# Optimization experiments

Hardware: AMD Instinct MI355X
Metric: run time of the kernel (lower is better)

Reference implementation:

```python
import jax, jax.numpy as jnp
import numpy as np

EPS = 1e-5
NUM_HEADS = 8
KEY_DEPTH = 128   # base_filters * key_expansion
VAL_DEPTH = 256   # base_filters * value_expansion
C_IN = 256


def conv1x1(x, w):
    # x: [N, Cin, L], w: [Cout, Cin] (1x1 conv, no bias)
    return jnp.einsum('oc,ncl->nol', w, x)


def group_norm1(x, w, b, eps=EPS):
    # torch GroupNorm(1, C) on [N, C, L]: normalize over (C, L) per sample,
    # per-channel affine.
    mu = jnp.mean(x, axis=(1, 2), keepdims=True)
    var = jnp.var(x, axis=(1, 2), keepdims=True)
    xn = (x - mu) * jax.lax.rsqrt(var + eps)
    return xn * w[None, :, None] + b[None, :, None]


def layer_norm_last2(x, eps=EPS):
    # freshly-constructed nn.LayerNorm([A, B]): weight=1, bias=0 -> pure norm
    mu = jnp.mean(x, axis=(-2, -1), keepdims=True)
    var = jnp.var(x, axis=(-2, -1), keepdims=True)
    return (x - mu) * jax.lax.rsqrt(var + eps)


def gelu(x):
    return jax.nn.gelu(x, approximate=False)  # torch F.gelu default (erf)


def setup_inputs() -> dict:
    key = jax.random.key(0)
    ks = jax.random.split(key, 16)
    N, L = 8, 1024
    qkv_out = 2 * KEY_DEPTH + VAL_DEPTH  # 512

    def w(k, shape, std=0.02):
        return jax.random.normal(k, shape, jnp.float32) * std

    def gw(k, c):
        return 1.0 + 0.1 * jax.random.normal(k, (c,), jnp.float32)

    return {
        'f': jax.random.normal(ks[0], (N, C_IN, L), jnp.float32),
        'w_z': w(ks[1], (C_IN, C_IN), np.sqrt(2.0 / C_IN)),
        'gz_w': gw(ks[2], C_IN), 'gz_b': w(ks[3], (C_IN,)),
        'w_qkv': w(ks[4], (qkv_out, C_IN), C_IN ** -0.5),
        'gq_w': gw(ks[5], qkv_out), 'gq_b': w(ks[6], (qkv_out,)),
        'w_out': w(ks[7], (C_IN, VAL_DEPTH), np.sqrt(2.0 / VAL_DEPTH)),
        'go_w': gw(ks[8], C_IN), 'go_b': w(ks[9], (C_IN,)),
        'w_ffn1': w(ks[10], (2 * C_IN, C_IN), np.sqrt(2.0 / C_IN)),
        'g1_w': gw(ks[11], 2 * C_IN), 'g1_b': w(ks[12], (2 * C_IN,)),
        'w_ffn2': w(ks[13], (C_IN, 2 * C_IN), np.sqrt(1.0 / C_IN)),
        'g2_w': gw(ks[14], C_IN), 'g2_b': w(ks[15], (C_IN,)),
    }


def reference(f, w_z, gz_w, gz_b, w_qkv, gq_w, gq_b, w_out, go_w, go_b,
              w_ffn1, g1_w, g1_b, w_ffn2, g2_w, g2_b):
    N, C, L = f.shape
    H = NUM_HEADS

    z = gelu(group_norm1(conv1x1(gelu(f), w_z), gz_w, gz_b))
    qkv = group_norm1(conv1x1(z, w_qkv), gq_w, gq_b)
    q, k, v = jnp.split(qkv, [KEY_DEPTH, 2 * KEY_DEPTH], axis=1)
    q = q.reshape(N, H, KEY_DEPTH // H, L)
    k = k.reshape(N, H, KEY_DEPTH // H, L)
    v = v.reshape(N, H, VAL_DEPTH // H, L)

    # [N, H, L, L] similarity, no scaling, then LayerNorm over full LxL map
    logits = jnp.einsum('nhcl,nhcm->nhlm', q, k)
    logits = layer_norm_last2(logits)

    # scatter-mask: diagonal -> -inf for every head
    eye = jnp.eye(L, dtype=bool)[None, None]  # [1,1,L,L]
    logits = jnp.where(eye, -jnp.inf, logits)

    attn = jax.nn.softmax(logits.astype(jnp.float32), axis=-1)
    attn = jnp.where(jnp.isnan(attn), 0.0, attn)

    out = jnp.einsum('nhlm,nhdm->nhdl', attn, v).reshape(N, VAL_DEPTH, L)
    out = gelu(layer_norm_last2(out))  # LayerNorm([C_v, L]), fresh params

    out = group_norm1(conv1x1(out, w_out), go_w, go_b)
    f = gelu(f + out)

    h = gelu(group_norm1(conv1x1(f, w_ffn1), g1_w, g1_b))
    h = group_norm1(conv1x1(h, w_ffn2), g2_w, g2_b)
    return gelu(f + h)
```

## Files before the change

kernel.cpp:

```cpp
#include <hip/hip_runtime.h>

#define LSEQ 1024

typedef __attribute__((ext_vector_type(8))) short bf16x8;
typedef __attribute__((ext_vector_type(4))) float f32x4;

__device__ __forceinline__ float gelu_f(float x){
    return 0.5f*x*(1.0f+erff(x*0.7071067811865476f));
}

__device__ __forceinline__ unsigned f2bf1(float x){
    unsigned u = __float_as_uint(x);
    return (u + 0x7fffu + ((u>>16)&1u)) >> 16;
}
__device__ __forceinline__ unsigned packbf(float lo, float hi){
    return f2bf1(lo) | (f2bf1(hi)<<16);
}

__global__ __launch_bounds__(256,2) void prologue(
    const float* __restrict__ w0, const float* __restrict__ w1,
    const float* __restrict__ w2, const float* __restrict__ w3,
    const float* __restrict__ w4, unsigned short* __restrict__ wdst,
    const float* __restrict__ f, unsigned short* __restrict__ t0,
    float* __restrict__ stats, float* __restrict__ covs)
{
    __shared__ float T[64][68];
    int b = blockIdx.x;
    int tid = threadIdx.x;

    if(b < 512){
        int ltile = (b&15)*64, ctile = ((b>>4)&3)*64, n = b>>6;
        const float* s = f + (size_t)n*256*LSEQ;
        int cl = tid>>4, l4 = (tid&15)*4;
        #pragma unroll
        for(int p=0;p<4;p++){
            int c_loc = p*16 + cl;
            float4 v = *(const float4*)&s[(size_t)(ctile+c_loc)*LSEQ + ltile + l4];
            float4 t;
            t.x = gelu_f(v.x); t.y = gelu_f(v.y); t.z = gelu_f(v.z); t.w = gelu_f(v.w);
            *(float4*)&T[c_loc][l4] = t;
        }
        __syncthreads();
        int l_loc = tid>>2, cg = (tid&3)*16;
        uint4 o0, o1;
        o0.x = packbf(T[cg+0][l_loc],  T[cg+1][l_loc]);
        o0.y = packbf(T[cg+2][l_loc],  T[cg+3][l_loc]);
        o0.z = packbf(T[cg+4][l_loc],  T[cg+5][l_loc]);
        o0.w = packbf(T[cg+6][l_loc],  T[cg+7][l_loc]);
        o1.x = packbf(T[cg+8][l_loc],  T[cg+9][l_loc]);
        o1.y = packbf(T[cg+10][l_loc], T[cg+11][l_loc]);
        o1.z = packbf(T[cg+12][l_loc], T[cg+13][l_loc]);
        o1.w = packbf(T[cg+14][l_loc], T[cg+15][l_loc]);
        unsigned short* d = t0 + (size_t)n*LSEQ*256 + (size_t)(ltile+l_loc)*256 + ctile + cg;
        *(uint4*)d = o0;
        *(uint4*)(d+8) = o1;
    } else if(b < 1024){
        int idx4 = (b-512)*256 + tid;
        const float* src; int off4;
        if(idx4 < 16384){ src=w0; off4=idx4; }
        else if(idx4 < 49152){ src=w1; off4=idx4-16384; }
        else if(idx4 < 65536){ src=w2; off4=idx4-49152; }
        else if(idx4 < 98304){ src=w3; off4=idx4-65536; }
        else { src=w4; off4=idx4-98304; }
        float4 v = ((const float4*)src)[off4];
        uint2 p; p.x = packbf(v.x,v.y); p.y = packbf(v.z,v.w);
        ((uint2*)wdst)[idx4] = p;
    } else if(b == 1024){
        if(tid < 64) ((float4*)stats)[tid] = (float4){0.f,0.f,0.f,0.f};
    } else {
        int i = (b-1025)*256 + tid;
        ((float4*)covs)[i] = (float4){0.f,0.f,0.f,0.f};
    }
}

__global__ __launch_bounds__(256,2) void xform_bf16(
    const float* __restrict__ src, const float* __restrict__ res,
    const float* __restrict__ stats,
    const float* __restrict__ gw, const float* __restrict__ gb,
    float cnt_inv, int C, unsigned short* __restrict__ dst)
{
    __shared__ float T[64][68];
    int n = blockIdx.z;
    int ltile = blockIdx.x*64, ctile = blockIdx.y*64;
    int tid = threadIdx.x;

    float mu=0.f, istd=1.f;
    if(stats){
        float s1 = stats[2*n], s2 = stats[2*n+1];
        mu = s1*cnt_inv;
        istd = rsqrtf(s2*cnt_inv - mu*mu + 1e-5f);
    }
    const float* s = src + (size_t)n*C*LSEQ;
    const float* r = res ? res + (size_t)n*C*LSEQ : nullptr;

    int cl = tid>>4, l4 = (tid&15)*4;
    #pragma unroll
    for(int p=0;p<4;p++){
        int c_loc = p*16 + cl;
        int c = ctile + c_loc;
        float w_ = 1.f, b_ = 0.f;
        if(stats){ w_ = istd; b_ = -mu*istd; }
        if(gw){ b_ = gb[c] + b_*gw[c]; w_ *= gw[c]; }
        float4 v = *(const float4*)&s[(size_t)c*LSEQ + ltile + l4];
        float4 t;
        t.x = v.x*w_+b_; t.y = v.y*w_+b_; t.z = v.z*w_+b_; t.w = v.w*w_+b_;
        if(r){
            float4 rv = *(const float4*)&r[(size_t)c*LSEQ + ltile + l4];
            t.x += rv.x; t.y += rv.y; t.z += rv.z; t.w += rv.w;
        }
        t.x = gelu_f(t.x); t.y = gelu_f(t.y); t.z = gelu_f(t.z); t.w = gelu_f(t.w);
        *(float4*)&T[c_loc][l4] = t;
    }
    __syncthreads();

    int l_loc = tid>>2, cg = (tid&3)*16;
    uint4 o0, o1;
    o0.x = packbf(T[cg+0][l_loc],  T[cg+1][l_loc]);
    o0.y = packbf(T[cg+2][l_loc],  T[cg+3][l_loc]);
    o0.z = packbf(T[cg+4][l_loc],  T[cg+5][l_loc]);
    o0.w = packbf(T[cg+6][l_loc],  T[cg+7][l_loc]);
    o1.x = packbf(T[cg+8][l_loc],  T[cg+9][l_loc]);
    o1.y = packbf(T[cg+10][l_loc], T[cg+11][l_loc]);
    o1.z = packbf(T[cg+12][l_loc], T[cg+13][l_loc]);
    o1.w = packbf(T[cg+14][l_loc], T[cg+15][l_loc]);
    unsigned short* d = dst + (size_t)n*LSEQ*C + (size_t)(ltile+l_loc)*C + ctile + cg;
    *(uint4*)d = o0;
    *(uint4*)(d+8) = o1;
}

__global__ __launch_bounds__(256,2) void gemm_bf16(
    const unsigned short* __restrict__ Abf,
    const unsigned short* __restrict__ Bbf,
    float* __restrict__ C,
    int M, int K,
    float* __restrict__ out_stats)
{
    __shared__ short As[64*264];
    __shared__ short Bs[64*264];

    int tid = threadIdx.x;
    int n = blockIdx.z, n0 = blockIdx.x*64, m0 = blockIdx.y*64;
    int wave = tid>>6, lane = tid&63;
    int col = lane&15, quad = lane>>4;
    int srow = tid>>2, sks = (tid&3)*8;

    const unsigned short* apt = Abf + (size_t)(m0+srow)*K + sks;
    const unsigned short* bpt = Bbf + ((size_t)n*LSEQ + n0+srow)*K + sks;

    f32x4 acc[4];
    #pragma unroll
    for(int t=0;t<4;t++) acc[t] = (f32x4){0.f,0.f,0.f,0.f};

    for(int kp=0; kp<K; kp+=256){
        __syncthreads();
        uint4 av[8], bw[8];
        #pragma unroll
        for(int i=0;i<8;i++) av[i] = *(const uint4*)(apt + kp + i*32);
        #pragma unroll
        for(int i=0;i<8;i++) bw[i] = *(const uint4*)(bpt + kp + i*32);
        #pragma unroll
        for(int i=0;i<8;i++) *(uint4*)&As[srow*264 + sks + i*32] = av[i];
        #pragma unroll
        for(int i=0;i<8;i++) *(uint4*)&Bs[srow*264 + sks + i*32] = bw[i];
        __syncthreads();

        #pragma unroll
        for(int kc=0;kc<8;kc++){
            bf16x8 af = *(bf16x8*)&As[(wave*16+col)*264 + kc*32 + quad*8];
            #pragma unroll
            for(int t=0;t<4;t++){
                bf16x8 bf = *(bf16x8*)&Bs[(t*16+col)*264 + kc*32 + quad*8];
                acc[t] = __builtin_amdgcn_mfma_f32_16x16x32_bf16(af, bf, acc[t], 0,0,0);
            }
        }
    }

    __syncthreads();
    size_t cbase = (size_t)n*M*LSEQ;
    float lsum=0.f, lsq=0.f;
    #pragma unroll
    for(int t=0;t<4;t++){
        #pragma unroll
        for(int r2=0;r2<4;r2++){
            int m = m0 + wave*16 + quad*4 + r2;
            int l = n0 + t*16 + col;
            float v = acc[t][r2];
            C[cbase + (size_t)m*LSEQ + l] = v;
            lsum += v; lsq += v*v;
        }
    }
    float* scr = (float*)As;
    scr[tid] = lsum; scr[256+tid] = lsq;
    __syncthreads();
    for(int s=128;s>0;s>>=1){
        if(tid<s){ scr[tid]+=scr[tid+s]; scr[256+tid]+=scr[256+tid+s]; }
        __syncthreads();
    }
    if(tid==0){
        atomicAdd(&out_stats[2*n],   scr[0]);
        atomicAdd(&out_stats[2*n+1], scr[256]);
    }
}

__global__ __launch_bounds__(256,2) void head_cov(
    const float* __restrict__ qkv,
    const float* __restrict__ s_qkv,
    const float* __restrict__ gq_w, const float* __restrict__ gq_b,
    float* __restrict__ covq, float* __restrict__ covk,
    float* __restrict__ sumq, float* __restrict__ sumk)
{
    __shared__ float Kq[16*132];
    __shared__ float Kk[16*132];
    int b = blockIdx.x;
    int head = b>>3, chunk = b&7;
    int n = head>>3, h = head&7;
    int tid = threadIdx.x;
    int m0 = chunk*128;

    float s1 = s_qkv[2*n], s2v = s_qkv[2*n+1];
    float mu  = s1*(1.f/524288.f);
    float var = s2v*(1.f/524288.f) - mu*mu;
    float istd = rsqrtf(var + 1e-5f);

    const float* base = qkv + (size_t)n*512*LSEQ;
    int m = tid&127, cg = tid>>7;
    #pragma unroll
    for(int cc=0;cc<8;cc++){
        int c = cg*8+cc;
        int chq = h*16+c, chk = 128+h*16+c;
        Kq[c*132+m] = (base[(size_t)chq*LSEQ+m0+m]-mu)*istd*gq_w[chq]+gq_b[chq];
        Kk[c*132+m] = (base[(size_t)chk*LSEQ+m0+m]-mu)*istd*gq_w[chk]+gq_b[chk];
    }
    __syncthreads();

    int i = tid>>4, j = tid&15;
    float q0=0,q1=0,q2=0,q3=0, k0=0,k1=0,k2=0,k3=0;
    for(int mm=0;mm<128;mm+=4){
        float4 qa = *(const float4*)&Kq[i*132+mm];
        float4 qb = *(const float4*)&Kq[j*132+mm];
        q0 += qa.x*qb.x; q1 += qa.y*qb.y; q2 += qa.z*qb.z; q3 += qa.w*qb.w;
        float4 ka = *(const float4*)&Kk[i*132+mm];
        float4 kb = *(const float4*)&Kk[j*132+mm];
        k0 += ka.x*kb.x; k1 += ka.y*kb.y; k2 += ka.z*kb.z; k3 += ka.w*kb.w;
    }
    atomicAdd(&covq[head*256 + i*16 + j], (q0+q1)+(q2+q3));
    atomicAdd(&covk[head*256 + i*16 + j], (k0+k1)+(k2+k3));

    if(i==0){
        float s=0.f;
        for(int mm=0;mm<128;mm+=4){
            float4 v = *(const float4*)&Kq[j*132+mm];
            s += (v.x+v.y)+(v.z+v.w);
        }
        atomicAdd(&sumq[head*16+j], s);
    }
    if(i==1){
        float s=0.f;
        for(int mm=0;mm<128;mm+=4){
            float4 v = *(const float4*)&Kk[j*132+mm];
            s += (v.x+v.y)+(v.z+v.w);
        }
        atomicAdd(&sumk[head*16+j], s);
    }
}

__global__ __launch_bounds__(256) void attn_kernel(
    const float* __restrict__ qkv,
    const float* __restrict__ s_qkv,
    const float* __restrict__ gq_w, const float* __restrict__ gq_b,
    const float* __restrict__ covq, const float* __restrict__ covk,
    const float* __restrict__ sumq, const float* __restrict__ sumk,
    float* __restrict__ out,
    float* __restrict__ out_stats)
{
    __shared__ short Qs[128*40];
    __shared__ short Ks[128*40];
    __shared__ short Vs[32*136];
    __shared__ short Ps[128*152];
    __shared__ float bounds_l[128];
    __shared__ float issum_l[128];
    __shared__ float sred4[4];

    int b = blockIdx.x;
    int head = b&63, rb = b>>6;
    int n = head>>3, h = head&7;
    int tid = threadIdx.x;
    int wv = tid>>6, lane = tid&63;
    int col = lane&15, quad = lane>>4;
    int l0 = rb*128;

    float ih;
    {
        float* fs = (float*)Ps;
        fs[tid] = covq[head*256+tid]*covk[head*256+tid];
        __syncthreads();
        for(int s=128;s>0;s>>=1){
            if(tid<s) fs[tid]+=fs[tid+s];
            __syncthreads();
        }
        if(tid==0){
            double S2 = (double)fs[0];
            double S1 = 0.0;
            for(int c=0;c<16;c++)
                S1 += (double)sumq[head*16+c]*(double)sumk[head*16+c];
            double cnt = 1048576.0;
            double mean = S1/cnt;
            double v2 = S2/cnt - mean*mean;
            if(v2 < 0.0) v2 = 0.0;
            fs[0] = (float)(1.0/sqrt(v2 + 1e-5));
        }
        __syncthreads();
        ih = fs[0];
        __syncthreads();
    }

    const float* base = qkv + (size_t)n*512*LSEQ;
    float s1 = s_qkv[2*n], s2v = s_qkv[2*n+1];
    float mu  = s1*(1.f/524288.f);
    float var = s2v*(1.f/524288.f) - mu*mu;
    float istd = rsqrtf(var + 1e-5f);

    {
        int row = tid>>1, hf = tid&1;
        uint4 z = {0,0,0,0};
        *(uint4*)&Qs[row*40 + 16 + hf*8] = z;
        *(uint4*)&Ks[row*40 + 16 + hf*8] = z;
    }

    {
        int row = tid>>1, cg = tid&1;
        float qn2p = 0.f;
        float qv[8];
        #pragma unroll
        for(int cc=0;cc<8;cc++){
            int ch = h*16 + cg*8 + cc;
            float w_ = gq_w[ch]*istd, b_ = gq_b[ch]-mu*istd*gq_w[ch];
            float x = base[(size_t)ch*LSEQ + l0 + row];
            float v = x*w_ + b_;
            qv[cc] = v;
            qn2p += v*v;
        }
        uint4 pq;
        pq.x = packbf(qv[0],qv[1]); pq.y = packbf(qv[2],qv[3]);
        pq.z = packbf(qv[4],qv[5]); pq.w = packbf(qv[6],qv[7]);
        *(uint4*)&Qs[row*40 + cg*8] = pq;
        float oth = __shfl_xor(qn2p, 1);
        if(cg==0) bounds_l[row] = sqrtf(qn2p + oth);
    }

    {
        float kn2max = 0.f;
        #pragma unroll
        for(int j=0;j<4;j++){
            int m = tid + j*256;
            float s = 0.f;
            for(int c=0;c<16;c++){
                int ch = 128+h*16+c;
                float x = base[(size_t)ch*LSEQ + m];
                float kv = (x-mu)*istd*gq_w[ch]+gq_b[ch];
                s += kv*kv;
            }
            kn2max = fmaxf(kn2max, s);
        }
        #pragma unroll
        for(int d=1;d<64;d<<=1) kn2max = fmaxf(kn2max, __shfl_xor(kn2max,d));
        if(lane==0) sred4[wv] = kn2max;
    }
    __syncthreads();
    float kmax = sqrtf(fmaxf(fmaxf(sred4[0],sred4[1]),fmaxf(sred4[2],sred4[3])));

    bf16x8 qf[2];
    float B2[2]; int grow[2];
    #pragma unroll
    for(int t=0;t<2;t++){
        int rl = (2*wv+t)*16 + col;
        qf[t] = *(bf16x8*)&Qs[rl*40 + quad*8];
        B2[t] = bounds_l[rl]*kmax*ih;
        grow[t] = l0 + rl;
    }

    int km_l = tid>>1, kg = tid&1;
    float kw8[8], kb8[8];
    #pragma unroll
    for(int cc=0;cc<8;cc++){
        int ch = 128+h*16+kg*8+cc;
        kw8[cc] = gq_w[ch]*istd;
        kb8[cc] = gq_b[ch]-mu*istd*gq_w[ch];
    }
    int vd = tid>>3, vmg = tid&7;
    float vw, vb;
    {
        int ch = 256+h*32+vd;
        vw = gq_w[ch]*istd;
        vb = gq_b[ch]-mu*istd*gq_w[ch];
    }
    const float* kp = base + (size_t)(128+h*16+kg*8)*LSEQ + km_l;
    const float* vp = base + (size_t)(256+h*32+vd)*LSEQ + vmg*16;

    f32x4 acc[2][2];
    #pragma unroll
    for(int t=0;t<2;t++){ acc[t][0]=(f32x4){0,0,0,0}; acc[t][1]=(f32x4){0,0,0,0}; }
    float ssum[2] = {0.f,0.f};
    const f32x4 zero4 = {0.f,0.f,0.f,0.f};

    for(int mc=0;mc<8;mc++){
        int M0 = mc*128;
        {
            float kv[8];
            #pragma unroll
            for(int cc=0;cc<8;cc++)
                kv[cc] = kp[(size_t)cc*LSEQ + M0]*kw8[cc] + kb8[cc];
            uint4 pk;
            pk.x=packbf(kv[0],kv[1]); pk.y=packbf(kv[2],kv[3]);
            pk.z=packbf(kv[4],kv[5]); pk.w=packbf(kv[6],kv[7]);
            *(uint4*)&Ks[km_l*40 + kg*8] = pk;
        }
        {
            float4 x0 = *(const float4*)&vp[M0];
            float4 x1 = *(const float4*)&vp[M0+4];
            float4 x2 = *(const float4*)&vp[M0+8];
            float4 x3 = *(const float4*)&vp[M0+12];
            uint4 p0, p1;
            p0.x = packbf(x0.x*vw+vb, x0.y*vw+vb);
            p0.y = packbf(x0.z*vw+vb, x0.w*vw+vb);
            p0.z = packbf(x1.x*vw+vb, x1.y*vw+vb);
            p0.w = packbf(x1.z*vw+vb, x1.w*vw+vb);
            p1.x = packbf(x2.x*vw+vb, x2.y*vw+vb);
            p1.y = packbf(x2.z*vw+vb, x2.w*vw+vb);
            p1.z = packbf(x3.x*vw+vb, x3.y*vw+vb);
            p1.w = packbf(x3.z*vw+vb, x3.w*vw+vb);
            *(uint4*)&Vs[vd*136 + vmg*16]     = p0;
            *(uint4*)&Vs[vd*136 + vmg*16 + 8] = p1;
        }
        __syncthreads();

        #pragma unroll
        for(int mt=0;mt<8;mt++){
            bf16x8 ak = *(bf16x8*)&Ks[(mt*16+col)*40 + quad*8];
            #pragma unroll
            for(int t=0;t<2;t++){
                f32x4 sc = __builtin_amdgcn_mfma_f32_16x16x32_bf16(ak, qf[t], zero4, 0,0,0);
                int mbase = M0 + mt*16 + quad*4;
                float pr[4];
                #pragma unroll
                for(int r=0;r<4;r++){
                    float e = __expf(fmaf(sc[r], ih, -B2[t]));
                    pr[r] = (mbase + r == grow[t]) ? 0.f : e;
                    ssum[t] += pr[r];
                }
                uint2 pw;
                pw.x = packbf(pr[0],pr[1]); pw.y = packbf(pr[2],pr[3]);
                *(uint2*)&Ps[((2*wv+t)*16+col)*152 + mt*16 + quad*4] = pw;
            }
        }
        #pragma unroll
        for(int kk=0;kk<4;kk++){
            bf16x8 bv0 = *(bf16x8*)&Vs[( col)*136 + kk*32 + quad*8];
            bf16x8 bv1 = *(bf16x8*)&Vs[((16+col))*136 + kk*32 + quad*8];
            #pragma unroll
            for(int t=0;t<2;t++){
                bf16x8 ap = *(bf16x8*)&Ps[((2*wv+t)*16+col)*152 + kk*32 + quad*8];
                acc[t][0] = __builtin_amdgcn_mfma_f32_16x16x32_bf16(ap, bv0, acc[t][0], 0,0,0);
                acc[t][1] = __builtin_amdgcn_mfma_f32_16x16x32_bf16(ap, bv1, acc[t][1], 0,0,0);
            }
        }
        __syncthreads();
    }

    #pragma unroll
    for(int t=0;t<2;t++){
        float v = ssum[t];
        v += __shfl_xor(v,16);
        v += __shfl_xor(v,32);
        if(quad==0) issum_l[(2*wv+t)*16+col] = v;
    }
    __syncthreads();
    if(tid<128) issum_l[tid] = 1.f/issum_l[tid];
    __syncthreads();

    float* ep = (float*)Ps;
    #pragma unroll
    for(int t=0;t<2;t++)
        #pragma unroll
        for(int dt=0;dt<2;dt++)
            *(f32x4*)&ep[(dt*16+col)*132 + (2*wv+t)*16 + quad*4] = acc[t][dt];
    __syncthreads();

    float lsum=0.f, lsq=0.f;
    size_t obase = (size_t)n*262144 + (size_t)h*32*LSEQ + l0;
    #pragma unroll
    for(int t=0;t<16;t++){
        int idx = t*256 + tid;
        int d = idx>>7, row = idx&127;
        float y = ep[d*132+row]*issum_l[row];
        out[obase + (size_t)d*LSEQ + row] = y;
        lsum += y; lsq += y*y;
    }
    float* red = (float*)Ks;
    red[tid]=lsum; red[256+tid]=lsq;
    __syncthreads();
    for(int s=128;s>0;s>>=1){
        if(tid<s){ red[tid]+=red[tid+s]; red[256+tid]+=red[256+tid+s]; }
        __syncthreads();
    }
    if(tid==0){
        atomicAdd(&out_stats[2*n],   red[0]);
        atomicAdd(&out_stats[2*n+1], red[256]);
    }
}

__global__ __launch_bounds__(256) void ew_final(
    const float* __restrict__ f, const float* __restrict__ x,
    const float* __restrict__ h2,
    const float* __restrict__ sx, const float* __restrict__ sh,
    const float* __restrict__ go_w, const float* __restrict__ go_b,
    const float* __restrict__ g2_w, const float* __restrict__ g2_b,
    float* __restrict__ out)
{
    int idx = blockIdx.x*256 + threadIdx.x;
    int n = idx >> 16;
    int c = (idx >> 8) & 255;
    float mux, isx, muh, ish;
    {
        float s1 = sx[2*n], s2 = sx[2*n+1];
        mux = s1*(1.f/262144.f);
        isx = rsqrtf(s2*(1.f/262144.f) - mux*mux + 1e-5f);
        float t1 = sh[2*n], t2 = sh[2*n+1];
        muh = t1*(1.f/262144.f);
        ish = rsqrtf(t2*(1.f/262144.f) - muh*muh + 1e-5f);
    }
    float wo = go_w[c]*isx, bo = go_b[c]-mux*isx*go_w[c];
    float w2 = g2_w[c]*ish, b2 = g2_b[c]-muh*ish*g2_w[c];
    float4 xv = ((const float4*)x)[idx];
    float4 fv = ((const float4*)f)[idx];
    float4 hv = ((const float4*)h2)[idx];
    float4 ov;
    float f1;
    f1 = gelu_f(fv.x + xv.x*wo+bo); ov.x = gelu_f(f1 + hv.x*w2+b2);
    f1 = gelu_f(fv.y + xv.y*wo+bo); ov.y = gelu_f(f1 + hv.y*w2+b2);
    f1 = gelu_f(fv.z + xv.z*wo+bo); ov.z = gelu_f(f1 + hv.z*w2+b2);
    f1 = gelu_f(fv.w + xv.w*wo+bo); ov.w = gelu_f(f1 + hv.w*w2+b2);
    ((float4*)out)[idx] = ov;
}

extern "C" void kernel_launch(void* const* d_in, const int* in_sizes, int n_in,
                              void* d_out, int out_size, void* d_ws, size_t ws_size,
                              hipStream_t stream) {
    const float* f     = (const float*)d_in[0];
    const float* w_z   = (const float*)d_in[1];
    const float* gz_w  = (const float*)d_in[2];
    const float* gz_b  = (const float*)d_in[3];
    const float* w_qkv = (const float*)d_in[4];
    const float* gq_w  = (const float*)d_in[5];
    const float* gq_b  = (const float*)d_in[6];
    const float* w_out = (const float*)d_in[7];
    const float* go_w  = (const float*)d_in[8];
    const float* go_b  = (const float*)d_in[9];
    const float* w_f1  = (const float*)d_in[10];
    const float* g1_w  = (const float*)d_in[11];
    const float* g1_b  = (const float*)d_in[12];
    const float* w_f2  = (const float*)d_in[13];
    const float* g2_w  = (const float*)d_in[14];
    const float* g2_b  = (const float*)d_in[15];

    float* ws = (float*)d_ws;
    float* stats = ws;
    float* s_z    = stats + 0;
    float* s_qkv  = stats + 16;
    float* s_attn = stats + 32;
    float* s_x    = stats + 48;
    float* s_h1   = stats + 64;
    float* s_h2   = stats + 80;

    float* qkvF = ws + 256;
    float* z0F  = qkvF + 4194304;
    float* xF   = z0F + 2097152;
    unsigned short* t0 = (unsigned short*)(xF + 2097152);
    unsigned short* t1 = t0 + 2097152;
    unsigned short* wp = t1 + 2097152;
    unsigned short* t4 = (unsigned short*)z0F;
    unsigned short* wp_z   = wp;
    unsigned short* wp_qkv = wp + 65536;
    unsigned short* wp_out = wp + 196608;
    unsigned short* wp_f1  = wp + 262144;
    unsigned short* wp_f2  = wp + 393216;

    float* covq = xF;
    float* covk = xF + 16384;
    float* sumq = xF + 32768;
    float* sumk = xF + 33792;

    float* outp = (float*)d_out;

    dim3 blk(256);
    prologue<<<1059,blk,0,stream>>>(w_z, w_qkv, w_out, w_f1, w_f2, wp,
        f, t0, stats, covq);
    gemm_bf16<<<dim3(16,4,8),blk,0,stream>>>(wp_z, t0, z0F, 256, 256, s_z);
    xform_bf16<<<dim3(16,4,8),blk,0,stream>>>(z0F, nullptr, s_z, gz_w, gz_b,
        1.f/262144.f, 256, t1);
    gemm_bf16<<<dim3(16,8,8),blk,0,stream>>>(wp_qkv, t1, qkvF, 512, 256, s_qkv);
    head_cov<<<512,blk,0,stream>>>(qkvF, s_qkv, gq_w, gq_b, covq, covk, sumq, sumk);
    attn_kernel<<<512,blk,0,stream>>>(qkvF, s_qkv, gq_w, gq_b,
        covq, covk, sumq, sumk, z0F, s_attn);
    xform_bf16<<<dim3(16,4,8),blk,0,stream>>>(z0F, nullptr, s_attn, nullptr, nullptr,
        1.f/262144.f, 256, t0);
    gemm_bf16<<<dim3(16,4,8),blk,0,stream>>>(wp_out, t0, xF, 256, 256, s_x);
    xform_bf16<<<dim3(16,4,8),blk,0,stream>>>(xF, f, s_x, go_w, go_b,
        1.f/262144.f, 256, t1);
    gemm_bf16<<<dim3(16,8,8),blk,0,stream>>>(wp_f1, t1, qkvF, 512, 256, s_h1);
    xform_bf16<<<dim3(16,8,8),blk,0,stream>>>(qkvF, nullptr, s_h1, g1_w, g1_b,
        1.f/524288.f, 512, t4);
    gemm_bf16<<<dim3(16,4,8),blk,0,stream>>>(wp_f2, t4, qkvF, 256, 512, s_h2);
    ew_final<<<2048,blk,0,stream>>>(f, xF, qkvF, s_x, s_h2,
        go_w, go_b, g2_w, g2_b, outp);
}
```

Before: 303.4 us.

## Use hardware bf16 pack, prefetch K/V tiles, wave-shuffle reductions, exp2 softmax

```diff
diff --git a/kernel.cpp b/kernel.cpp
--- a/kernel.cpp
+++ b/kernel.cpp
@@ -9,12 +9,10 @@
     return 0.5f*x*(1.0f+erff(x*0.7071067811865476f));
 }
 
-__device__ __forceinline__ unsigned f2bf1(float x){
-    unsigned u = __float_as_uint(x);
-    return (u + 0x7fffu + ((u>>16)&1u)) >> 16;
-}
-__device__ __forceinline__ unsigned packbf(float lo, float hi){
-    return f2bf1(lo) | (f2bf1(hi)<<16);
+__device__ __forceinline__ unsigned cvtpk(float lo, float hi){
+    unsigned r;
+    asm("v_cvt_pk_bf16_f32 %0, %1, %2" : "=v"(r) : "v"(lo), "v"(hi));
+    return r;
 }
 
 __global__ __launch_bounds__(256,2) void prologue(
@@ -43,14 +41,14 @@
         __syncthreads();
         int l_loc = tid>>2, cg = (tid&3)*16;
         uint4 o0, o1;
-        o0.x = packbf(T[cg+0][l_loc],  T[cg+1][l_loc]);
-        o0.y = packbf(T[cg+2][l_loc],  T[cg+3][l_loc]);
-        o0.z = packbf(T[cg+4][l_loc],  T[cg+5][l_loc]);
-        o0.w = packbf(T[cg+6][l_loc],  T[cg+7][l_loc]);
-        o1.x = packbf(T[cg+8][l_loc],  T[cg+9][l_loc]);
-        o1.y = packbf(T[cg+10][l_loc], T[cg+11][l_loc]);
-        o1.z = packbf(T[cg+12][l_loc], T[cg+13][l_loc]);
-        o1.w = packbf(T[cg+14][l_loc], T[cg+15][l_loc]);
+        o0.x = cvtpk(T[cg+0][l_loc],  T[cg+1][l_loc]);
+        o0.y = cvtpk(T[cg+2][l_loc],  T[cg+3][l_loc]);
+        o0.z = cvtpk(T[cg+4][l_loc],  T[cg+5][l_loc]);
+        o0.w = cvtpk(T[cg+6][l_loc],  T[cg+7][l_loc]);
+        o1.x = cvtpk(T[cg+8][l_loc],  T[cg+9][l_loc]);
+        o1.y = cvtpk(T[cg+10][l_loc], T[cg+11][l_loc]);
+        o1.z = cvtpk(T[cg+12][l_loc], T[cg+13][l_loc]);
+        o1.w = cvtpk(T[cg+14][l_loc], T[cg+15][l_loc]);
         unsigned short* d = t0 + (size_t)n*LSEQ*256 + (size_t)(ltile+l_loc)*256 + ctile + cg;
         *(uint4*)d = o0;
         *(uint4*)(d+8) = o1;
@@ -63,7 +61,7 @@
         else if(idx4 < 98304){ src=w3; off4=idx4-65536; }
         else { src=w4; off4=idx4-98304; }
         float4 v = ((const float4*)src)[off4];
-        uint2 p; p.x = packbf(v.x,v.y); p.y = packbf(v.z,v.w);
+        uint2 p; p.x = cvtpk(v.x,v.y); p.y = cvtpk(v.z,v.w);
         ((uint2*)wdst)[idx4] = p;
     } else if(b == 1024){
         if(tid < 64) ((float4*)stats)[tid] = (float4){0.f,0.f,0.f,0.f};
@@ -115,14 +113,14 @@
 
     int l_loc = tid>>2, cg = (tid&3)*16;
     uint4 o0, o1;
-    o0.x = packbf(T[cg+0][l_loc],  T[cg+1][l_loc]);
-    o0.y = packbf(T[cg+2][l_loc],  T[cg+3][l_loc]);
-    o0.z = packbf(T[cg+4][l_loc],  T[cg+5][l_loc]);
-    o0.w = packbf(T[cg+6][l_loc],  T[cg+7][l_loc]);
-    o1.x = packbf(T[cg+8][l_loc],  T[cg+9][l_loc]);
-    o1.y = packbf(T[cg+10][l_loc], T[cg+11][l_loc]);
-    o1.z = packbf(T[cg+12][l_loc], T[cg+13][l_loc]);
-    o1.w = packbf(T[cg+14][l_loc], T[cg+15][l_loc]);
+    o0.x = cvtpk(T[cg+0][l_loc],  T[cg+1][l_loc]);
+    o0.y = cvtpk(T[cg+2][l_loc],  T[cg+3][l_loc]);
+    o0.z = cvtpk(T[cg+4][l_loc],  T[cg+5][l_loc]);
+    o0.w = cvtpk(T[cg+6][l_loc],  T[cg+7][l_loc]);
+    o1.x = cvtpk(T[cg+8][l_loc],  T[cg+9][l_loc]);
+    o1.y = cvtpk(T[cg+10][l_loc], T[cg+11][l_loc]);
+    o1.z = cvtpk(T[cg+12][l_loc], T[cg+13][l_loc]);
+    o1.w = cvtpk(T[cg+14][l_loc], T[cg+15][l_loc]);
     unsigned short* d = dst + (size_t)n*LSEQ*C + (size_t)(ltile+l_loc)*C + ctile + cg;
     *(uint4*)d = o0;
     *(uint4*)(d+8) = o1;
@@ -175,7 +173,6 @@
         }
     }
 
-    __syncthreads();
     size_t cbase = (size_t)n*M*LSEQ;
     float lsum=0.f, lsq=0.f;
     #pragma unroll
@@ -189,16 +186,14 @@
             lsum += v; lsq += v*v;
         }
     }
-    float* scr = (float*)As;
-    scr[tid] = lsum; scr[256+tid] = lsq;
-    __syncthreads();
-    for(int s=128;s>0;s>>=1){
-        if(tid<s){ scr[tid]+=scr[tid+s]; scr[256+tid]+=scr[256+tid+s]; }
-        __syncthreads();
-    }
-    if(tid==0){
-        atomicAdd(&out_stats[2*n],   scr[0]);
-        atomicAdd(&out_stats[2*n+1], scr[256]);
+    #pragma unroll
+    for(int d=1;d<64;d<<=1){
+        lsum += __shfl_xor(lsum, d);
+        lsq  += __shfl_xor(lsq,  d);
+    }
+    if(lane==0){
+        atomicAdd(&out_stats[2*n],   lsum);
+        atomicAdd(&out_stats[2*n+1], lsq);
     }
 }
 
@@ -291,15 +286,14 @@
 
     float ih;
     {
-        float* fs = (float*)Ps;
-        fs[tid] = covq[head*256+tid]*covk[head*256+tid];
-        __syncthreads();
-        for(int s=128;s>0;s>>=1){
-            if(tid<s) fs[tid]+=fs[tid+s];
-            __syncthreads();
-        }
+        float prod = covq[head*256+tid]*covk[head*256+tid];
+        #pragma unroll
+        for(int d=1;d<64;d<<=1) prod += __shfl_xor(prod, d);
+        if(lane==0) sred4[wv] = prod;
+        __syncthreads();
         if(tid==0){
-            double S2 = (double)fs[0];
+            double S2 = (double)sred4[0] + (double)sred4[1]
+                      + (double)sred4[2] + (double)sred4[3];
             double S1 = 0.0;
             for(int c=0;c<16;c++)
                 S1 += (double)sumq[head*16+c]*(double)sumk[head*16+c];
@@ -307,12 +301,13 @@
             double mean = S1/cnt;
             double v2 = S2/cnt - mean*mean;
             if(v2 < 0.0) v2 = 0.0;
-            fs[0] = (float)(1.0/sqrt(v2 + 1e-5));
-        }
-        __syncthreads();
-        ih = fs[0];
-        __syncthreads();
-    }
+            sred4[0] = (float)(1.0/sqrt(v2 + 1e-5));
+        }
+        __syncthreads();
+        ih = sred4[0];
+        __syncthreads();
+    }
+    float ihl = ih * 1.4426950408889634f;
 
     const float* base = qkv + (size_t)n*512*LSEQ;
     float s1 = s_qkv[2*n], s2v = s_qkv[2*n+1];
@@ -341,8 +336,8 @@
             qn2p += v*v;
         }
         uint4 pq;
-        pq.x = packbf(qv[0],qv[1]); pq.y = packbf(qv[2],qv[3]);
-        pq.z = packbf(qv[4],qv[5]); pq.w = packbf(qv[6],qv[7]);
+        pq.x = cvtpk(qv[0],qv[1]); pq.y = cvtpk(qv[2],qv[3]);
+        pq.z = cvtpk(qv[4],qv[5]); pq.w = cvtpk(qv[6],qv[7]);
         *(uint4*)&Qs[row*40 + cg*8] = pq;
         float oth = __shfl_xor(qn2p, 1);
         if(cg==0) bounds_l[row] = sqrtf(qn2p + oth);
@@ -370,12 +365,12 @@
     float kmax = sqrtf(fmaxf(fmaxf(sred4[0],sred4[1]),fmaxf(sred4[2],sred4[3])));
 
     bf16x8 qf[2];
-    float B2[2]; int grow[2];
+    float B2l[2]; int grow[2];
     #pragma unroll
     for(int t=0;t<2;t++){
         int rl = (2*wv+t)*16 + col;
         qf[t] = *(bf16x8*)&Qs[rl*40 + quad*8];
-        B2[t] = bounds_l[rl]*kmax*ih;
+        B2l[t] = bounds_l[rl]*kmax*ihl;
         grow[t] = l0 + rl;
     }
 
@@ -403,53 +398,71 @@
     float ssum[2] = {0.f,0.f};
     const f32x4 zero4 = {0.f,0.f,0.f,0.f};
 
+    float kn[8];
+    float4 v0n, v1n, v2n, v3n;
+    #pragma unroll
+    for(int cc=0;cc<8;cc++) kn[cc] = kp[(size_t)cc*LSEQ];
+    v0n = *(const float4*)&vp[0];
+    v1n = *(const float4*)&vp[4];
+    v2n = *(const float4*)&vp[8];
+    v3n = *(const float4*)&vp[12];
+
     for(int mc=0;mc<8;mc++){
         int M0 = mc*128;
         {
-            float kv[8];
-            #pragma unroll
-            for(int cc=0;cc<8;cc++)
-                kv[cc] = kp[(size_t)cc*LSEQ + M0]*kw8[cc] + kb8[cc];
             uint4 pk;
-            pk.x=packbf(kv[0],kv[1]); pk.y=packbf(kv[2],kv[3]);
-            pk.z=packbf(kv[4],kv[5]); pk.w=packbf(kv[6],kv[7]);
+            pk.x = cvtpk(kn[0]*kw8[0]+kb8[0], kn[1]*kw8[1]+kb8[1]);
+            pk.y = cvtpk(kn[2]*kw8[2]+kb8[2], kn[3]*kw8[3]+kb8[3]);
+            pk.z = cvtpk(kn[4]*kw8[4]+kb8[4], kn[5]*kw8[5]+kb8[5]);
+            pk.w = cvtpk(kn[6]*kw8[6]+kb8[6], kn[7]*kw8[7]+kb8[7]);
             *(uint4*)&Ks[km_l*40 + kg*8] = pk;
         }
         {
-            float4 x0 = *(const float4*)&vp[M0];
-            float4 x1 = *(const float4*)&vp[M0+4];
-            float4 x2 = *(const float4*)&vp[M0+8];
-            float4 x3 = *(const float4*)&vp[M0+12];
             uint4 p0, p1;
-            p0.x = packbf(x0.x*vw+vb, x0.y*vw+vb);
-            p0.y = packbf(x0.z*vw+vb, x0.w*vw+vb);
-            p0.z = packbf(x1.x*vw+vb, x1.y*vw+vb);
-            p0.w = packbf(x1.z*vw+vb, x1.w*vw+vb);
-            p1.x = packbf(x2.x*vw+vb, x2.y*vw+vb);
-            p1.y = packbf(x2.z*vw+vb, x2.w*vw+vb);
-            p1.z = packbf(x3.x*vw+vb, x3.y*vw+vb);
-            p1.w = packbf(x3.z*vw+vb, x3.w*vw+vb);
+            p0.x = cvtpk(v0n.x*vw+vb, v0n.y*vw+vb);
+            p0.y = cvtpk(v0n.z*vw+vb, v0n.w*vw+vb);
+            p0.z = cvtpk(v1n.x*vw+vb, v1n.y*vw+vb);
+            p0.w = cvtpk(v1n.z*vw+vb, v1n.w*vw+vb);
+            p1.x = cvtpk(v2n.x*vw+vb, v2n.y*vw+vb);
+            p1.y = cvtpk(v2n.z*vw+vb, v2n.w*vw+vb);
+            p1.z = cvtpk(v3n.x*vw+vb, v3n.y*vw+vb);
+            p1.w = cvtpk(v3n.z*vw+vb, v3n.w*vw+vb);
             *(uint4*)&Vs[vd*136 + vmg*16]     = p0;
             *(uint4*)&Vs[vd*136 + vmg*16 + 8] = p1;
         }
         __syncthreads();
 
+        if(mc < 7){
+            int M1 = M0 + 128;
+            #pragma unroll
+            for(int cc=0;cc<8;cc++) kn[cc] = kp[(size_t)cc*LSEQ + M1];
+            v0n = *(const float4*)&vp[M1];
+            v1n = *(const float4*)&vp[M1+4];
+            v2n = *(const float4*)&vp[M1+8];
+            v3n = *(const float4*)&vp[M1+12];
+        }
+
+        __builtin_amdgcn_s_setprio(1);
+        bool diag_mc = (mc == rb);
         #pragma unroll
         for(int mt=0;mt<8;mt++){
             bf16x8 ak = *(bf16x8*)&Ks[(mt*16+col)*40 + quad*8];
             #pragma unroll
             for(int t=0;t<2;t++){
                 f32x4 sc = __builtin_amdgcn_mfma_f32_16x16x32_bf16(ak, qf[t], zero4, 0,0,0);
-                int mbase = M0 + mt*16 + quad*4;
                 float pr[4];
                 #pragma unroll
-                for(int r=0;r<4;r++){
-                    float e = __expf(fmaf(sc[r], ih, -B2[t]));
-                    pr[r] = (mbase + r == grow[t]) ? 0.f : e;
-                    ssum[t] += pr[r];
+                for(int r=0;r<4;r++)
+                    pr[r] = exp2f(fmaf(sc[r], ihl, -B2l[t]));
+                if(diag_mc){
+                    int mbase = M0 + mt*16 + quad*4;
+                    #pragma unroll
+                    for(int r=0;r<4;r++)
+                        if(mbase + r == grow[t]) pr[r] = 0.f;
                 }
+                ssum[t] += (pr[0]+pr[1])+(pr[2]+pr[3]);
                 uint2 pw;
-                pw.x = packbf(pr[0],pr[1]); pw.y = packbf(pr[2],pr[3]);
+                pw.x = cvtpk(pr[0],pr[1]); pw.y = cvtpk(pr[2],pr[3]);
                 *(uint2*)&Ps[((2*wv+t)*16+col)*152 + mt*16 + quad*4] = pw;
             }
         }
@@ -464,6 +477,7 @@
                 acc[t][1] = __builtin_amdgcn_mfma_f32_16x16x32_bf16(ap, bv1, acc[t][1], 0,0,0);
             }
         }
+        __builtin_amdgcn_s_setprio(0);
         __syncthreads();
     }
 
@@ -496,16 +510,14 @@
         out[obase + (size_t)d*LSEQ + row] = y;
         lsum += y; lsq += y*y;
     }
-    float* red = (float*)Ks;
-    red[tid]=lsum; red[256+tid]=lsq;
-    __syncthreads();
-    for(int s=128;s>0;s>>=1){
-        if(tid<s){ red[tid]+=red[tid+s]; red[256+tid]+=red[256+tid+s]; }
-        __syncthreads();
-    }
-    if(tid==0){
-        atomicAdd(&out_stats[2*n],   red[0]);
-        atomicAdd(&out_stats[2*n+1], red[256]);
+    #pragma unroll
+    for(int d=1;d<64;d<<=1){
+        lsum += __shfl_xor(lsum, d);
+        lsq  += __shfl_xor(lsq,  d);
+    }
+    if(lane==0){
+        atomicAdd(&out_stats[2*n],   lsum);
+        atomicAdd(&out_stats[2*n+1], lsq);
     }
 }
 
```

New measurement: 608.3 us. 2x slower.
